# Performance work log

Hardware: AMD Instinct MI355X
Metric: run time of the kernel (lower is better)

Reference implementation:

```python
import jax, jax.numpy as jnp
import numpy as np

N_NODES = 100000
N_EDGES = 1600000
N_GRAPHS = 1000
NODES_PER_GRAPH = 100  # batch vector is arange(N)//100: exactly 100 nodes per graph
HID = 32
MAX_Z = 1000
K = 30
D_LAT = HID * 3 + 1  # 97, total_latent_dim


def setup_inputs() -> dict:
    key = jax.random.key(0)
    ks = jax.random.split(key, 24)
    s = 1.0 / np.sqrt(HID)
    inp = {
        "z": jax.random.randint(ks[0], (N_NODES,), 0, MAX_Z, dtype=jnp.int32),
        "edge_index": jax.random.randint(ks[1], (2, N_EDGES), 0, N_NODES, dtype=jnp.int32),
        "batch": (jnp.arange(N_NODES, dtype=jnp.int32) // NODES_PER_GRAPH),
        "edge_weight": jax.random.uniform(ks[2], (N_EDGES,), jnp.float32, 0.1, 1.0),
        "z_emb": jax.random.normal(ks[3], (MAX_Z, HID), jnp.float32) * 0.1,
        # GCNConv stack: [32->32, 32->32, 32->32, 32->1]
        "Wg1": jax.random.normal(ks[4], (HID, HID)) * s,
        "bg1": jnp.zeros((HID,), jnp.float32),
        "Wg2": jax.random.normal(ks[5], (HID, HID)) * s,
        "bg2": jnp.zeros((HID,), jnp.float32),
        "Wg3": jax.random.normal(ks[6], (HID, HID)) * s,
        "bg3": jnp.zeros((HID,), jnp.float32),
        "Wg4": jax.random.normal(ks[7], (HID, 1)) * s,
        "bg4": jnp.zeros((1,), jnp.float32),
        # Conv1d(1, 16, kernel=97, stride=97)
        "Wc1": jax.random.normal(ks[8], (16, D_LAT)) * (1.0 / np.sqrt(D_LAT)),
        "bc1": jnp.zeros((16,), jnp.float32),
        # Conv1d(16, 32, kernel=5, stride=1)
        "Wc2": jax.random.normal(ks[9], (32, 16, 5)) * (1.0 / np.sqrt(16 * 5)),
        "bc2": jnp.zeros((32,), jnp.float32),
        # Linear(352, 128), Linear(128, 1)
        "Wl1": jax.random.normal(ks[10], (352, 128)) * (1.0 / np.sqrt(352)),
        "bl1": jnp.zeros((128,), jnp.float32),
        "Wl2": jax.random.normal(ks[11], (128, 1)) * (1.0 / np.sqrt(128)),
        "bl2": jnp.zeros((1,), jnp.float32),
    }
    return inp


def gcn_conv(x, src, dst, ew, W, b, n):
    # PyG GCNConv: xW, add self-loops (weight 1), sym-normalize, aggregate at dst, + bias
    xw = x @ W
    deg = jax.ops.segment_sum(ew, dst, num_segments=n) + 1.0  # +1 for self loop
    dinv = jnp.where(deg > 0, jax.lax.rsqrt(deg), 0.0)
    norm = dinv[src] * ew * dinv[dst]                          # [E]
    out = jax.ops.segment_sum(norm[:, None] * xw[src], dst, num_segments=n)
    out = out + xw * (dinv * dinv)[:, None]                    # self-loop term
    return out + b


def _forward(z, edge_index, batch, edge_weight, z_emb, Wg1, bg1, Wg2, bg2, Wg3, bg3,
             Wg4, bg4, Wc1, bc1, Wc2, bc2, Wl1, bl1, Wl2, bl2):
    src, dst = edge_index[0], edge_index[1]
    n = z.shape[0]
    x = z_emb[z]                                              # [N, 32]
    xs = []
    h = x
    for W, b in ((Wg1, bg1), (Wg2, bg2), (Wg3, bg3), (Wg4, bg4)):
        h = jnp.tanh(gcn_conv(h, src, dst, edge_weight, W, b, n))
        xs.append(h)
    x = jnp.concatenate(xs, axis=-1)                          # [N, 97]
    # global_sort_pool: batch is uniform (100 nodes/graph) so dense batching is a reshape
    dense = x.reshape(N_GRAPHS, NODES_PER_GRAPH, D_LAT)       # [B, 100, 97]
    idx = jnp.argsort(-dense[:, :, -1], axis=1)[:, :K]        # sort desc by last channel
    top = jnp.take_along_axis(dense, idx[:, :, None], axis=1)  # [B, 30, 97]
    # Conv1d(1,16,97,stride=97) on flattened [B,1,30*97] == per-slot dense layer
    y = jax.nn.relu(jnp.einsum('bkd,cd->bck', top, Wc1) + bc1[None, :, None])  # [B,16,30]
    y = y.reshape(N_GRAPHS, 16, K // 2, 2).max(axis=-1)        # MaxPool1d(2,2) -> [B,16,15]
    y = jax.lax.conv_general_dilated(y, Wc2, (1,), 'VALID',
                                     dimension_numbers=('NCH', 'OIH', 'NCH'))
    y = jax.nn.relu(y + bc2[None, :, None])                    # [B,32,11]
    y = y.reshape(N_GRAPHS, -1)                                # [B,352]
    y = jax.nn.relu(y @ Wl1 + bl1)                             # dropout: eval mode, identity
    return y @ Wl2 + bl2                                       # [B,1]


def reference(z, edge_index, batch, edge_weight, z_emb, Wg1, bg1, Wg2, bg2, Wg3, bg3,
              Wg4, bg4, Wc1, bc1, Wc2, bc2, Wl1, bl1, Wl2, bl2):
    return _forward(z, edge_index, batch, edge_weight, z_emb, Wg1, bg1, Wg2, bg2, Wg3,
                    bg3, Wg4, bg4, Wc1, bc1, Wc2, bc2, Wl1, bl1, Wl2, bl2)
```

## Files before the change

### kernel.cpp

```cpp
#include <hip/hip_runtime.h>

#define HID 32
#define DLAT 97
#define NPG 100
#define TOPK 30
#define BKT_NODES 128
#define BKT_SHIFT 7
#define NBUCK 1024
#define CAPF 2432
#define CHUNK 8192

typedef float f32x4 __attribute__((ext_vector_type(4)));

__device__ __forceinline__ f32x4 gload4(const float* p) {
    f32x4 r;
    asm volatile("global_load_dwordx4 %0, %1, off" : "=v"(r) : "v"(p));
    return r;
}

__global__ __launch_bounds__(256) void binB1_kernel(
    const int* __restrict__ src, const int* __restrict__ dst,
    const float* __restrict__ ew, int* __restrict__ gcursor,
    int2* __restrict__ bedge, int E) {
    __shared__ int hist[NBUCK];
    __shared__ int lcur[NBUCK];
    __shared__ int dcache[CHUNK];
    for (int i = threadIdx.x; i < NBUCK; i += 256) hist[i] = 0;
    __syncthreads();
    int base = blockIdx.x * CHUNK;
    int M = min(E - base, CHUNK);
    for (int i = threadIdx.x; i < M; i += 256) {
        int d = dst[base + i];
        dcache[i] = d;
        atomicAdd(&hist[d >> BKT_SHIFT], 1);
    }
    __syncthreads();
    for (int b = threadIdx.x; b < NBUCK; b += 256) {
        int v = hist[b];
        lcur[b] = b * CAPF + (v ? atomicAdd(&gcursor[b], v) : 0);
    }
    __syncthreads();
    for (int i = threadIdx.x; i < M; i += 256) {
        int d = dcache[i];
        int slot = atomicAdd(&lcur[d >> BKT_SHIFT], 1);
        bedge[slot] = make_int2(src[base + i] | ((d & (BKT_NODES - 1)) << 20),
                                __float_as_int(ew[base + i]));
    }
}

__global__ __launch_bounds__(256) void scan1024_kernel(
    const int* __restrict__ g, int* __restrict__ bstart) {
    __shared__ int sh[256];
    int t = threadIdx.x;
    int t4 = t * 4;
    int a0 = g[t4], a1 = g[t4 + 1], a2 = g[t4 + 2], a3 = g[t4 + 3];
    int tsum = a0 + a1 + a2 + a3;
    sh[t] = tsum;
    __syncthreads();
    for (int off = 1; off < 256; off <<= 1) {
        int tv = (t >= off) ? sh[t - off] : 0;
        __syncthreads();
        sh[t] += tv;
        __syncthreads();
    }
    int e = sh[t] - tsum;
    bstart[t4] = e;
    bstart[t4 + 1] = e + a0;
    bstart[t4 + 2] = e + a0 + a1;
    bstart[t4 + 3] = e + a0 + a1 + a2;
}

__global__ __launch_bounds__(256) void sortlocal3_kernel(
    const int2* __restrict__ bedge, const int* __restrict__ gcursor,
    const int* __restrict__ bstart,
    const int* __restrict__ z, const float* __restrict__ z_emb,
    const float* __restrict__ W1, int2* __restrict__ csr,
    int* __restrict__ row_start, int* __restrict__ row_deg,
    float* __restrict__ dinv, float* __restrict__ xw_a, int N) {
    __shared__ int2 LDSe[CAPF];
    __shared__ int cnt[BKT_NODES];
    __shared__ int sh2[BKT_NODES];
    __shared__ int lc2[BKT_NODES];
    __shared__ int zloc[BKT_NODES];
    __shared__ float wsum[BKT_NODES];
    __shared__ float dloc[BKT_NODES];
    __shared__ float W1L[HID * HID];

    int b = blockIdx.x, t = threadIdx.x;
    for (int i = t; i < HID * HID; i += 256) W1L[i] = W1[i];
    if (t < BKT_NODES) { cnt[t] = 0; wsum[t] = 0.f; }
    __syncthreads();

    const int begOut = bstart[b];
    const int M = gcursor[b];

    for (int i = t; i < M; i += 256) {
        int2 e = bedge[(size_t)b * CAPF + i];
        LDSe[i] = e;
        int nl = (e.x >> 20) & (BKT_NODES - 1);
        atomicAdd(&cnt[nl], 1);
        atomicAdd(&wsum[nl], __int_as_float(e.y));
    }
    __syncthreads();
    int v = 0, excl = 0;
    int n = b * BKT_NODES + t;
    if (t < BKT_NODES) { v = cnt[t]; sh2[t] = v; }
    __syncthreads();
    for (int off = 1; off < BKT_NODES; off <<= 1) {
        int tv = (t >= off && t < BKT_NODES) ? sh2[t - off] : 0;
        __syncthreads();
        if (t < BKT_NODES) sh2[t] += tv;
        __syncthreads();
    }
    if (t < BKT_NODES) {
        excl = sh2[t] - v;
        lc2[t] = excl;
        float di = 1.f / sqrtf(1.f + wsum[t]);
        dloc[t] = di;
        if (n < N) {
            row_start[n] = begOut + excl;
            row_deg[n] = v;
            dinv[n] = di;
            zloc[t] = z[n];
        } else {
            zloc[t] = 0;
        }
    }
    __syncthreads();
    for (int i = t; i < M; i += 256) {
        int2 e = LDSe[i];
        int slot = atomicAdd(&lc2[(e.x >> 20) & (BKT_NODES - 1)], 1);
        csr[begOut + slot] = make_int2(e.x & 0xFFFFF, e.y);
    }
    int lim = min(BKT_NODES, N - b * BKT_NODES);
    if (lim > 0) {
        for (int idx = t; idx < lim * HID; idx += 256) {
            int nl = idx >> 5, f = idx & 31;
            const float* row = z_emb + (size_t)zloc[nl] * HID;
            float s = 0.f;
#pragma unroll
            for (int k = 0; k < HID; ++k) s += row[k] * W1L[k * HID + f];
            xw_a[(size_t)(b * BKT_NODES + nl) * HID + f] = s * dloc[nl];
        }
    }
}

template <int MODE>
__global__ __launch_bounds__(256) void agg32y_kernel(
    const int* __restrict__ row_start, const int* __restrict__ row_deg,
    const int2* __restrict__ csr, const float* __restrict__ xw,
    const float* __restrict__ b, const float* __restrict__ dinv,
    const float* __restrict__ Wn, float* __restrict__ cout,
    float* __restrict__ xw_next, int N) {
    __shared__ float WnL[HID * HID];
    int t = threadIdx.x;
    if (MODE == 0) {
        for (int i = t; i < HID * HID; i += 256) WnL[i] = Wn[i];
    } else {
        if (t < HID) WnL[t] = Wn[t];
    }
    __syncthreads();
    int tid = blockIdx.x * 256 + t;
    int n = tid >> 5;
    if (n >= N) return;
    int lane = t & 31;
    int eq = lane & 3;
    int f4 = lane & 28;
    int beg = row_start[n];
    int deg = row_deg[n];
    float di = dinv[n];
    float selfv = xw[(size_t)n * HID + lane];
    int end = beg + deg;
    float4 acc = make_float4(0.f, 0.f, 0.f, 0.f);
    for (int i = beg; i < end; i += 32) {
        int e = i + lane;
        int2 ce = csr[min(e, end - 1)];
        float we = (e < end) ? __int_as_float(ce.y) : 0.f;
        int ci = ce.x;
        f32x4 x[8];
        float w[8];
#pragma unroll
        for (int j = 0; j < 8; ++j) {
            int s = 4 * j + eq;
            int idx = __shfl(ci, s, 32);
            w[j] = __shfl(we, s, 32);
            x[j] = gload4(xw + (size_t)idx * HID + f4);
        }
        asm volatile("s_waitcnt vmcnt(0)" ::: "memory");
        __builtin_amdgcn_sched_barrier(0);
#pragma unroll
        for (int j = 0; j < 8; ++j) {
            acc.x += w[j] * x[j].x;
            acc.y += w[j] * x[j].y;
            acc.z += w[j] * x[j].z;
            acc.w += w[j] * x[j].w;
        }
    }
#pragma unroll
    for (int m = 1; m <= 2; m <<= 1) {
        acc.x += __shfl_xor(acc.x, m, 32);
        acc.y += __shfl_xor(acc.y, m, 32);
        acc.z += __shfl_xor(acc.z, m, 32);
        acc.w += __shfl_xor(acc.w, m, 32);
    }
    float s = (eq == 0) ? acc.x : (eq == 1) ? acc.y : (eq == 2) ? acc.z : acc.w;
    float outv = tanhf(di * (s + selfv) + b[lane]);
    cout[(size_t)n * HID + lane] = outv;

    if (MODE == 0) {
        float p = 0.f;
#pragma unroll
        for (int k = 0; k < HID; ++k) {
            float ok = __shfl(outv, k, 32);
            p += ok * WnL[k * HID + lane];
        }
        xw_next[(size_t)n * HID + lane] = p * di;
    } else {
        float p = outv * WnL[lane];
        p += __shfl_xor(p, 16, 32);
        p += __shfl_xor(p, 8, 32);
        p += __shfl_xor(p, 4, 32);
        p += __shfl_xor(p, 2, 32);
        p += __shfl_xor(p, 1, 32);
        if (lane == 0) xw_next[n] = p * di;
    }
}

__global__ __launch_bounds__(256) void topk_head_kernel(
    const int* __restrict__ row_start, const int* __restrict__ row_deg,
    const int2* __restrict__ csr, const float* __restrict__ xw4,
    const float* __restrict__ b4, const float* __restrict__ dinv,
    const float* __restrict__ cblk,
    const float* __restrict__ Wc1, const float* __restrict__ bc1,
    const float* __restrict__ Wc2, const float* __restrict__ bc2,
    const float* __restrict__ Wl1, const float* __restrict__ bl1,
    const float* __restrict__ Wl2, const float* __restrict__ bl2,
    float* __restrict__ out, int N) {
    int g = blockIdx.x;
    int tid = threadIdx.x;
    __shared__ float v[NPG];
    __shared__ int tidx[TOPK];
    __shared__ float tval[TOPK];
    __shared__ float top[TOPK * DLAT];
    __shared__ float Wc1L[16 * DLAT];
    __shared__ float Wc2L[32 * 16 * 5];
    __shared__ float y1[16 * TOPK];
    __shared__ float y2[16 * 15];
    __shared__ float y3[352];
    __shared__ float r[256];

    for (int i = tid; i < 16 * DLAT; i += 256) Wc1L[i] = Wc1[i];
    for (int i = tid; i < 32 * 16 * 5; i += 256) Wc2L[i] = Wc2[i];

    if (tid < NPG) {
        int n = g * NPG + tid;
        int beg = row_start[n], end = beg + row_deg[n];
        float s0 = 0.f, s1 = 0.f;
        for (int i = beg; i < end; i += 4) {
            int2 e0 = csr[min(i, end - 1)];
            int2 e1 = csr[min(i + 1, end - 1)];
            int2 e2 = csr[min(i + 2, end - 1)];
            int2 e3 = csr[min(i + 3, end - 1)];
            float x0 = xw4[e0.x], x1 = xw4[e1.x], x2 = xw4[e2.x], x3 = xw4[e3.x];
            s0 += __int_as_float(e0.y) * x0;
            if (i + 1 < end) s1 += __int_as_float(e1.y) * x1;
            if (i + 2 < end) s0 += __int_as_float(e2.y) * x2;
            if (i + 3 < end) s1 += __int_as_float(e3.y) * x3;
        }
        v[tid] = tanhf(dinv[n] * ((s0 + s1) + xw4[n]) + b4[0]);
    }
    __syncthreads();
    if (tid < NPG) {
        float vi = v[tid];
        int cnt = 0;
#pragma unroll 4
        for (int j = 0; j < NPG; ++j) {
            float vj = v[j];
            cnt += (vj > vi) || (vj == vi && j < tid);
        }
        if (cnt < TOPK) {
            tidx[cnt] = g * NPG + tid;
            tval[cnt] = vi;
        }
    }
    __syncthreads();

    for (int idx = tid; idx < TOPK * DLAT; idx += 256) {
        int k = idx / DLAT, d = idx - k * DLAT;
        float val;
        if (d == 96) val = tval[k];
        else val = cblk[(size_t)(d >> 5) * N * HID + (size_t)tidx[k] * HID + (d & 31)];
        top[idx] = val;
    }
    __syncthreads();

    for (int idx = tid; idx < 16 * TOPK; idx += 256) {
        int c = idx / TOPK, k = idx % TOPK;
        float s = bc1[c];
        const float* w = Wc1L + c * DLAT;
        const float* t = top + k * DLAT;
#pragma unroll 4
        for (int d = 0; d < DLAT; ++d) s += t[d] * w[d];
        y1[c * TOPK + k] = fmaxf(s, 0.f);
    }
    __syncthreads();

    for (int idx = tid; idx < 16 * 15; idx += 256) {
        int c = idx / 15, j = idx % 15;
        y2[idx] = fmaxf(y1[c * TOPK + 2 * j], y1[c * TOPK + 2 * j + 1]);
    }
    __syncthreads();

    for (int idx = tid; idx < 352; idx += 256) {
        int o = idx / 11, t = idx % 11;
        float s = bc2[o];
#pragma unroll
        for (int i = 0; i < 16; ++i) {
#pragma unroll
            for (int k = 0; k < 5; ++k)
                s += Wc2L[(o * 16 + i) * 5 + k] * y2[i * 15 + t + k];
        }
        y3[idx] = fmaxf(s, 0.f);
    }
    __syncthreads();

    {
        int half = tid >> 7;
        int o = tid & 127;
        int d0 = half * 176;
        float s = (half == 0) ? bl1[o] : 0.f;
#pragma unroll 1
        for (int d = d0; d < d0 + 176; d += 8) {
            float wv[8], yv[8];
#pragma unroll
            for (int j = 0; j < 8; ++j) wv[j] = Wl1[(d + j) * 128 + o];
#pragma unroll
            for (int j = 0; j < 8; ++j) yv[j] = y3[d + j];
#pragma unroll
            for (int j = 0; j < 8; ++j) s += yv[j] * wv[j];
        }
        r[tid] = s;
    }
    __syncthreads();
    if (tid < 128) r[tid] = fmaxf(r[tid] + r[tid + 128], 0.f) * Wl2[tid];
    __syncthreads();
    if (tid < 64) r[tid] += r[tid + 64];
    __syncthreads();
    if (tid == 0) {
        float s = 0.f;
        for (int j = 0; j < 64; ++j) s += r[j];
        out[g] = s + bl2[0];
    }
}


extern "C" void kernel_launch(void* const* d_in, const int* in_sizes, int n_in,
                              void* d_out, int out_size, void* d_ws, size_t ws_size,
                              hipStream_t stream) {
    const int* z = (const int*)d_in[0];
    const int* ei = (const int*)d_in[1];
    const float* ew = (const float*)d_in[3];
    const float* z_emb = (const float*)d_in[4];
    const float* Wg[4] = {(const float*)d_in[5], (const float*)d_in[7],
                          (const float*)d_in[9], (const float*)d_in[11]};
    const float* bg[4] = {(const float*)d_in[6], (const float*)d_in[8],
                          (const float*)d_in[10], (const float*)d_in[12]};
    const float* Wc1 = (const float*)d_in[13];
    const float* bc1 = (const float*)d_in[14];
    const float* Wc2 = (const float*)d_in[15];
    const float* bc2 = (const float*)d_in[16];
    const float* Wl1 = (const float*)d_in[17];
    const float* bl1 = (const float*)d_in[18];
    const float* Wl2 = (const float*)d_in[19];
    const float* bl2 = (const float*)d_in[20];
    float* out = (float*)d_out;

    const int N = in_sizes[0];
    const int E = in_sizes[1] / 2;
    const int G = out_size;
    const int* src = ei;
    const int* dst = ei + E;

    auto cdiv = [](long long a, long long b) { return (int)((a + b - 1) / b); };
    const int NB = cdiv(E, CHUNK);
    const int NBKT = cdiv(N, BKT_NODES);

    char* ws = (char*)d_ws;
    int2* bedge = (int2*)ws;                  ws += sizeof(int2) * (size_t)NBUCK * CAPF;
    int2* csr = (int2*)ws;                    ws += sizeof(int2) * (size_t)E;
    int* gcursor = (int*)ws;                  ws += sizeof(int) * NBUCK;
    int* bstart = (int*)ws;                   ws += sizeof(int) * NBUCK;
    int* row_start = (int*)ws;                ws += sizeof(int) * N;
    int* row_deg = (int*)ws;                  ws += sizeof(int) * N;
    float* dinv = (float*)ws;                 ws += sizeof(float) * N;
    float* xw_a = (float*)ws;                 ws += sizeof(float) * (size_t)N * HID;
    float* cblk = (float*)ws;                 ws += sizeof(float) * (size_t)3 * N * HID;
    float* xw4 = (float*)ws;                  ws += sizeof(float) * N;
    float* xw_b = (float*)bedge;
    float* cb0 = cblk;
    float* cb1 = cblk + (size_t)N * HID;
    float* cb2 = cblk + (size_t)2 * N * HID;

    const int B = 256;

    hipMemsetAsync(gcursor, 0, sizeof(int) * NBUCK, stream);
    binB1_kernel<<<NB, B, 0, stream>>>(src, dst, ew, gcursor, bedge, E);
    scan1024_kernel<<<1, B, 0, stream>>>(gcursor, bstart);
    sortlocal3_kernel<<<NBKT, B, 0, stream>>>(bedge, gcursor, bstart, z, z_emb, Wg[0],
                                              csr, row_start, row_deg, dinv, xw_a, N);

    const int AGGB = cdiv((long long)N * 32, B);
    agg32y_kernel<0><<<AGGB, B, 0, stream>>>(row_start, row_deg, csr, xw_a, bg[0], dinv,
                                             Wg[1], cb0, xw_b, N);
    agg32y_kernel<0><<<AGGB, B, 0, stream>>>(row_start, row_deg, csr, xw_b, bg[1], dinv,
                                             Wg[2], cb1, xw_a, N);
    agg32y_kernel<1><<<AGGB, B, 0, stream>>>(row_start, row_deg, csr, xw_a, bg[2], dinv,
                                             Wg[3], cb2, xw4, N);

    topk_head_kernel<<<G, 256, 0, stream>>>(row_start, row_deg, csr, xw4, bg[3], dinv,
                                            cblk, Wc1, bc1, Wc2, bc2, Wl1, bl1,
                                            Wl2, bl2, out, N);
}
```

Measured before the change: 371.5 us.

## Skip empty gather slots in aggregation, widen bin/sort blocks, vectorize top-k gather

The aggregation kernel now computes how many 4-edge groups in each 32-edge chunk hold real edges, and skips the shuffles, gathers and FMAs for empty groups. With a mean degree near 16, about half the gathers were padding. The binning and local-sort kernels now launch 512 threads per block instead of 256. The top-k feature copy in the head kernel uses float4 loads instead of scalar loads. The extra branch on jmax may make the load schedule less regular, and larger blocks lower the number of resident blocks per CU.

```diff
diff --git a/kernel.cpp b/kernel.cpp
--- a/kernel.cpp
+++ b/kernel.cpp
@@ -18,29 +18,29 @@
     return r;
 }
 
-__global__ __launch_bounds__(256) void binB1_kernel(
+__global__ __launch_bounds__(512) void binB1_kernel(
     const int* __restrict__ src, const int* __restrict__ dst,
     const float* __restrict__ ew, int* __restrict__ gcursor,
     int2* __restrict__ bedge, int E) {
     __shared__ int hist[NBUCK];
     __shared__ int lcur[NBUCK];
     __shared__ int dcache[CHUNK];
-    for (int i = threadIdx.x; i < NBUCK; i += 256) hist[i] = 0;
+    for (int i = threadIdx.x; i < NBUCK; i += 512) hist[i] = 0;
     __syncthreads();
     int base = blockIdx.x * CHUNK;
     int M = min(E - base, CHUNK);
-    for (int i = threadIdx.x; i < M; i += 256) {
+    for (int i = threadIdx.x; i < M; i += 512) {
         int d = dst[base + i];
         dcache[i] = d;
         atomicAdd(&hist[d >> BKT_SHIFT], 1);
     }
     __syncthreads();
-    for (int b = threadIdx.x; b < NBUCK; b += 256) {
+    for (int b = threadIdx.x; b < NBUCK; b += 512) {
         int v = hist[b];
         lcur[b] = b * CAPF + (v ? atomicAdd(&gcursor[b], v) : 0);
     }
     __syncthreads();
-    for (int i = threadIdx.x; i < M; i += 256) {
+    for (int i = threadIdx.x; i < M; i += 512) {
         int d = dcache[i];
         int slot = atomicAdd(&lcur[d >> BKT_SHIFT], 1);
         bedge[slot] = make_int2(src[base + i] | ((d & (BKT_NODES - 1)) << 20),
@@ -70,7 +70,7 @@
     bstart[t4 + 3] = e + a0 + a1 + a2;
 }
 
-__global__ __launch_bounds__(256) void sortlocal3_kernel(
+__global__ __launch_bounds__(512) void sortlocal3_kernel(
     const int2* __restrict__ bedge, const int* __restrict__ gcursor,
     const int* __restrict__ bstart,
     const int* __restrict__ z, const float* __restrict__ z_emb,
@@ -87,14 +87,14 @@
     __shared__ float W1L[HID * HID];
 
     int b = blockIdx.x, t = threadIdx.x;
-    for (int i = t; i < HID * HID; i += 256) W1L[i] = W1[i];
+    for (int i = t; i < HID * HID; i += 512) W1L[i] = W1[i];
     if (t < BKT_NODES) { cnt[t] = 0; wsum[t] = 0.f; }
     __syncthreads();
 
     const int begOut = bstart[b];
     const int M = gcursor[b];
 
-    for (int i = t; i < M; i += 256) {
+    for (int i = t; i < M; i += 512) {
         int2 e = bedge[(size_t)b * CAPF + i];
         LDSe[i] = e;
         int nl = (e.x >> 20) & (BKT_NODES - 1);
@@ -127,14 +127,14 @@
         }
     }
     __syncthreads();
-    for (int i = t; i < M; i += 256) {
+    for (int i = t; i < M; i += 512) {
         int2 e = LDSe[i];
         int slot = atomicAdd(&lc2[(e.x >> 20) & (BKT_NODES - 1)], 1);
         csr[begOut + slot] = make_int2(e.x & 0xFFFFF, e.y);
     }
     int lim = min(BKT_NODES, N - b * BKT_NODES);
     if (lim > 0) {
-        for (int idx = t; idx < lim * HID; idx += 256) {
+        for (int idx = t; idx < lim * HID; idx += 512) {
             int nl = idx >> 5, f = idx & 31;
             const float* row = z_emb + (size_t)zloc[nl] * HID;
             float s = 0.f;
@@ -146,7 +146,7 @@
 }
 
 template <int MODE>
-__global__ __launch_bounds__(256) void agg32y_kernel(
+__global__ __launch_bounds__(256) void agg32z_kernel(
     const int* __restrict__ row_start, const int* __restrict__ row_deg,
     const int2* __restrict__ csr, const float* __restrict__ xw,
     const float* __restrict__ b, const float* __restrict__ dinv,
@@ -177,23 +177,28 @@
         int2 ce = csr[min(e, end - 1)];
         float we = (e < end) ? __int_as_float(ce.y) : 0.f;
         int ci = ce.x;
+        int jmax = min(8, (end - i + 3) >> 2);
         f32x4 x[8];
         float w[8];
 #pragma unroll
         for (int j = 0; j < 8; ++j) {
-            int s = 4 * j + eq;
-            int idx = __shfl(ci, s, 32);
-            w[j] = __shfl(we, s, 32);
-            x[j] = gload4(xw + (size_t)idx * HID + f4);
+            if (j < jmax) {
+                int s = 4 * j + eq;
+                int idx = __shfl(ci, s, 32);
+                w[j] = __shfl(we, s, 32);
+                x[j] = gload4(xw + (size_t)idx * HID + f4);
+            }
         }
         asm volatile("s_waitcnt vmcnt(0)" ::: "memory");
         __builtin_amdgcn_sched_barrier(0);
 #pragma unroll
         for (int j = 0; j < 8; ++j) {
-            acc.x += w[j] * x[j].x;
-            acc.y += w[j] * x[j].y;
-            acc.z += w[j] * x[j].z;
-            acc.w += w[j] * x[j].w;
+            if (j < jmax) {
+                acc.x += w[j] * x[j].x;
+                acc.y += w[j] * x[j].y;
+                acc.z += w[j] * x[j].z;
+                acc.w += w[j] * x[j].w;
+            }
         }
     }
 #pragma unroll
@@ -285,13 +290,15 @@
     }
     __syncthreads();
 
-    for (int idx = tid; idx < TOPK * DLAT; idx += 256) {
-        int k = idx / DLAT, d = idx - k * DLAT;
-        float val;
-        if (d == 96) val = tval[k];
-        else val = cblk[(size_t)(d >> 5) * N * HID + (size_t)tidx[k] * HID + (d & 31)];
-        top[idx] = val;
-    }
+    for (int idx = tid; idx < TOPK * 24; idx += 256) {
+        int k = idx / 24, q = idx - k * 24;
+        int l = q >> 3, fq = q & 7;
+        const float4 val =
+            *(const float4*)(cblk + (size_t)l * N * HID + (size_t)tidx[k] * HID + fq * 4);
+        float* dst = top + k * DLAT + l * HID + fq * 4;
+        dst[0] = val.x; dst[1] = val.y; dst[2] = val.z; dst[3] = val.w;
+    }
+    if (tid < TOPK) top[tid * DLAT + 96] = tval[tid];
     __syncthreads();
 
     for (int idx = tid; idx < 16 * TOPK; idx += 256) {
@@ -401,21 +408,19 @@
     float* cb1 = cblk + (size_t)N * HID;
     float* cb2 = cblk + (size_t)2 * N * HID;
 
-    const int B = 256;
-
     hipMemsetAsync(gcursor, 0, sizeof(int) * NBUCK, stream);
-    binB1_kernel<<<NB, B, 0, stream>>>(src, dst, ew, gcursor, bedge, E);
-    scan1024_kernel<<<1, B, 0, stream>>>(gcursor, bstart);
-    sortlocal3_kernel<<<NBKT, B, 0, stream>>>(bedge, gcursor, bstart, z, z_emb, Wg[0],
-                                              csr, row_start, row_deg, dinv, xw_a, N);
-
-    const int AGGB = cdiv((long long)N * 32, B);
-    agg32y_kernel<0><<<AGGB, B, 0, stream>>>(row_start, row_deg, csr, xw_a, bg[0], dinv,
-                                             Wg[1], cb0, xw_b, N);
-    agg32y_kernel<0><<<AGGB, B, 0, stream>>>(row_start, row_deg, csr, xw_b, bg[1], dinv,
-                                             Wg[2], cb1, xw_a, N);
-    agg32y_kernel<1><<<AGGB, B, 0, stream>>>(row_start, row_deg, csr, xw_a, bg[2], dinv,
-                                             Wg[3], cb2, xw4, N);
+    binB1_kernel<<<NB, 512, 0, stream>>>(src, dst, ew, gcursor, bedge, E);
+    scan1024_kernel<<<1, 256, 0, stream>>>(gcursor, bstart);
+    sortlocal3_kernel<<<NBKT, 512, 0, stream>>>(bedge, gcursor, bstart, z, z_emb, Wg[0],
+                                                csr, row_start, row_deg, dinv, xw_a, N);
+
+    const int AGGB = cdiv((long long)N * 32, 256);
+    agg32z_kernel<0><<<AGGB, 256, 0, stream>>>(row_start, row_deg, csr, xw_a, bg[0],
+                                               dinv, Wg[1], cb0, xw_b, N);
+    agg32z_kernel<0><<<AGGB, 256, 0, stream>>>(row_start, row_deg, csr, xw_b, bg[1],
+                                               dinv, Wg[2], cb1, xw_a, N);
+    agg32z_kernel<1><<<AGGB, 256, 0, stream>>>(row_start, row_deg, csr, xw_a, bg[2],
+                                               dinv, Wg[3], cb2, xw4, N);
 
     topk_head_kernel<<<G, 256, 0, stream>>>(row_start, row_deg, csr, xw4, bg[3], dinv,
                                             cblk, Wc1, bc1, Wc2, bc2, Wl1, bl1,
```

Result: faster. 346.8 us, median of 2 (-6.6%).
